# Optimization experiments

Measured on AMD Instinct MI355X. Metric: run time of the kernel, lower is better.

The kernel has to match this reference:

```python
import jax, jax.numpy as jnp
import numpy as np

OUT, IN = 11008, 4096
GROUP = 128
NUM_GROUPS = IN // GROUP  # 32
PACKED = OUT * IN // 2
TOKENS = 4096


def setup_inputs() -> dict:
    key = jax.random.key(0)
    k1, k2, k3, k4 = jax.random.split(key, 4)
    x = jax.random.normal(k1, (TOKENS, IN), dtype=jnp.float32)
    # packed bytes: two int4 values per byte (low nibble = even index)
    w_packed = jax.random.randint(k2, (PACKED,), 0, 256, dtype=jnp.int32)
    # per-(out_channel, group) scale and integer zero-point
    w_scale = jax.random.uniform(k3, (OUT, NUM_GROUPS), dtype=jnp.float32) * 0.02 + 1e-3
    w_zero = jax.random.randint(k4, (OUT, NUM_GROUPS), 0, 16, dtype=jnp.int32)
    return {"x": x, "w_packed": w_packed, "w_scale": w_scale, "w_zero": w_zero}


def _dequant_weight(w_packed, w_scale, w_zero):
    out_features, num_groups = w_scale.shape
    in_features = (w_packed.shape[0] * 2) // out_features
    group = in_features // num_groups
    # unpack nibbles: element 2i -> low nibble, element 2i+1 -> high nibble
    low = w_packed & 15
    high = (w_packed >> 4) & 15
    w4 = jnp.stack([low, high], axis=-1).reshape(out_features, in_features)
    # signed int4: values >= 8 map to value - 16
    w4 = jnp.where(w4 >= 8, w4 - 16, w4).astype(jnp.float32)
    # per-group dequant: (w - zero) * scale
    wg = w4.reshape(out_features, num_groups, group)
    w = (wg - w_zero.astype(jnp.float32)[:, :, None]) * w_scale[:, :, None]
    return w.reshape(out_features, in_features)


def reference(x, w_packed, w_scale, w_zero):
    w = _dequant_weight(w_packed, w_scale, w_zero)  # [OUT, IN]
    return x @ w.T  # [TOKENS, OUT]
```

## Files before the change

kernel.cpp:

```cpp
#include <hip/hip_runtime.h>
#include <hip/hip_bf16.h>
#include <stdint.h>
#include <stddef.h>


#define M_TOK 4096
#define K_IN  4096
#define N_OUT 11008
#define QGROUPS 32

typedef __bf16 bf8 __attribute__((ext_vector_type(8)));
typedef short  s8v __attribute__((ext_vector_type(8)));
typedef float  f4v __attribute__((ext_vector_type(4)));

__device__ __forceinline__ unsigned short f2bf(float f) {
  union { float f; unsigned u; } v; v.f = f;
  unsigned r = v.u + 0x7FFFu + ((v.u >> 16) & 1u);
  return (unsigned short)(r >> 16);
}

__device__ __forceinline__ void gload16(const void* g, void* l) {
  __builtin_amdgcn_global_load_lds(
      (__attribute__((address_space(1))) void*)(g),
      (__attribute__((address_space(3))) void*)(l),
      16, 0, 0);
}

__global__ __launch_bounds__(256) void cvt_x_kernel(const float* __restrict__ x,
                                                    unsigned short* __restrict__ xb) {
  size_t t = (size_t)blockIdx.x * 256 + threadIdx.x;
  const float4* src = (const float4*)x + t * 2;
  float4 a = src[0], b = src[1];
  union { unsigned short u[8]; s8v v; } o;
  o.u[0] = f2bf(a.x); o.u[1] = f2bf(a.y); o.u[2] = f2bf(a.z); o.u[3] = f2bf(a.w);
  o.u[4] = f2bf(b.x); o.u[5] = f2bf(b.y); o.u[6] = f2bf(b.z); o.u[7] = f2bf(b.w);
  ((s8v*)xb)[t] = o.v;
}

__device__ __forceinline__ void deq_pair(int b, float s, float zf, unsigned short* dst) {
  int lo = (b << 28) >> 28;
  int hi = (b << 24) >> 28;
  dst[0] = f2bf(((float)lo - zf) * s);
  dst[1] = f2bf(((float)hi - zf) * s);
}

__global__ __launch_bounds__(256) void deq_w_kernel(const int* __restrict__ wp,
                                                    const float* __restrict__ wsc,
                                                    const int* __restrict__ wz,
                                                    unsigned short* __restrict__ wb) {
  size_t t = (size_t)blockIdx.x * 256 + threadIdx.x;
  size_t e0 = t * 8;
  int o = (int)(e0 >> 12);
  int k = (int)(e0 & 4095);
  int g = k >> 7;
  float s  = wsc[o * QGROUPS + g];
  float zf = (float)wz[o * QGROUPS + g];
  int4 pk = ((const int4*)wp)[t];
  union { unsigned short u[8]; s8v v; } r;
  deq_pair(pk.x, s, zf, &r.u[0]);
  deq_pair(pk.y, s, zf, &r.u[2]);
  deq_pair(pk.z, s, zf, &r.u[4]);
  deq_pair(pk.w, s, zf, &r.u[6]);
  ((s8v*)wb)[t] = r.v;
}

template <bool PRE>
__global__ __launch_bounds__(256, 2) void gemm_kernel(
    const unsigned short* __restrict__ Ab,
    const unsigned short* __restrict__ Bb,
    const float* __restrict__ X,
    const int* __restrict__ WP,
    const float* __restrict__ WS,
    const int* __restrict__ WZ,
    float* __restrict__ C) {
  __shared__ __align__(16) short As[128 * 64];
  __shared__ __align__(16) short Bs[128 * 64];

  const int tid  = threadIdx.x;
  const int lane = tid & 63;
  const int wid  = tid >> 6;
  const int n0 = blockIdx.x * 128;
  const int m0 = blockIdx.y * 128;
  const int wm = (wid >> 1) * 64;
  const int wn = (wid & 1) * 64;
  const int quad = lane >> 4;
  const int lrow = lane & 15;
  const int sw   = lrow & 7;

  f4v acc[4][4];
#pragma unroll
  for (int i = 0; i < 4; ++i)
#pragma unroll
    for (int j = 0; j < 4; ++j) acc[i][j] = (f4v){0.f, 0.f, 0.f, 0.f};

  const int srl = lane >> 3;
  const int skb = (lane & 7) ^ srl;
  const int frow  = tid >> 1;
  const int fhalf = tid & 1;

  for (int kt = 0; kt < K_IN / 64; ++kt) {
    const int k0 = kt * 64;
    __syncthreads();
    if (PRE) {
#pragma unroll
      for (int j = 0; j < 4; ++j) {
        int slab = wid * 4 + j;
        int row  = slab * 8 + srl;
        gload16(Ab + (size_t)(m0 + row) * K_IN + k0 + skb * 8,
                (char*)As + slab * 1024);
        gload16(Bb + (size_t)(n0 + row) * K_IN + k0 + skb * 8,
                (char*)Bs + slab * 1024);
      }
    } else {
      const int g = k0 >> 7;
      float s  = WS[(n0 + frow) * QGROUPS + g];
      float zf = (float)WZ[(n0 + frow) * QGROUPS + g];
#pragma unroll
      for (int j = 0; j < 4; ++j) {
        int kb = fhalf * 4 + j;
        int unit = frow * 8 + (kb ^ (frow & 7));
        const float4* xs = (const float4*)(X + (size_t)(m0 + frow) * K_IN + k0 + kb * 8);
        float4 a = xs[0], b = xs[1];
        union { unsigned short u[8]; s8v v; } oa;
        oa.u[0] = f2bf(a.x); oa.u[1] = f2bf(a.y); oa.u[2] = f2bf(a.z); oa.u[3] = f2bf(a.w);
        oa.u[4] = f2bf(b.x); oa.u[5] = f2bf(b.y); oa.u[6] = f2bf(b.z); oa.u[7] = f2bf(b.w);
        *(s8v*)(As + unit * 8) = oa.v;
        const int4 pk = *(const int4*)(WP + ((size_t)(n0 + frow) * K_IN + k0 + kb * 8) / 2);
        union { unsigned short u[8]; s8v v; } ob;
        deq_pair(pk.x, s, zf, &ob.u[0]);
        deq_pair(pk.y, s, zf, &ob.u[2]);
        deq_pair(pk.z, s, zf, &ob.u[4]);
        deq_pair(pk.w, s, zf, &ob.u[6]);
        *(s8v*)(Bs + unit * 8) = ob.v;
      }
    }
    __syncthreads();

#pragma unroll
    for (int ks = 0; ks < 2; ++ks) {
      bf8 af[4], bfr[4];
#pragma unroll
      for (int mi = 0; mi < 4; ++mi) {
        int row = wm + mi * 16 + lrow;
        int unit = row * 8 + ((ks * 4 + quad) ^ sw);
        af[mi] = *reinterpret_cast<const bf8*>(&As[unit * 8]);
      }
#pragma unroll
      for (int ni = 0; ni < 4; ++ni) {
        int row = wn + ni * 16 + lrow;
        int unit = row * 8 + ((ks * 4 + quad) ^ sw);
        bfr[ni] = *reinterpret_cast<const bf8*>(&Bs[unit * 8]);
      }
#pragma unroll
      for (int mi = 0; mi < 4; ++mi)
#pragma unroll
        for (int ni = 0; ni < 4; ++ni)
          acc[mi][ni] = __builtin_amdgcn_mfma_f32_16x16x32_bf16(
              af[mi], bfr[ni], acc[mi][ni], 0, 0, 0);
    }
  }

#pragma unroll
  for (int mi = 0; mi < 4; ++mi) {
#pragma unroll
    for (int r = 0; r < 4; ++r) {
      int m = m0 + wm + mi * 16 + quad * 4 + r;
      float* crow = C + (size_t)m * N_OUT + n0 + wn + lrow;
#pragma unroll
      for (int ni = 0; ni < 4; ++ni) crow[ni * 16] = acc[mi][ni][r];
    }
  }
}

extern "C" void kernel_launch(void* const* d_in, const int* in_sizes, int n_in,
                              void* d_out, int out_size, void* d_ws, size_t ws_size,
                              hipStream_t stream) {
  const float* x   = (const float*)d_in[0];
  const int*   wp  = (const int*)d_in[1];
  const float* wsc = (const float*)d_in[2];
  const int*   wz  = (const int*)d_in[3];
  float* out = (float*)d_out;

  const size_t needA = (size_t)M_TOK * K_IN * sizeof(unsigned short);
  const size_t needB = (size_t)N_OUT * K_IN * sizeof(unsigned short);
  dim3 grid(N_OUT / 128, M_TOK / 128);

  if (ws_size >= needA + needB) {
    unsigned short* Ab = (unsigned short*)d_ws;
    unsigned short* Bb = (unsigned short*)((char*)d_ws + needA);
    cvt_x_kernel<<<(M_TOK * (size_t)K_IN) / (8 * 256), 256, 0, stream>>>(x, Ab);
    deq_w_kernel<<<((size_t)N_OUT * K_IN) / (8 * 256), 256, 0, stream>>>(wp, wsc, wz, Bb);
    gemm_kernel<true><<<grid, 256, 0, stream>>>(Ab, Bb, nullptr, nullptr, nullptr, nullptr, out);
  } else {
    gemm_kernel<false><<<grid, 256, 0, stream>>>(nullptr, nullptr, x, wp, wsc, wz, out);
  }
}
```

Before: 751.7 us.

## Switch to fp16 MFMA with in-GEMM int4 dequant and grouped tile order

Replaces the bf16 prepass pipeline. Activations are converted to fp16 with a permuted element order, and the weights are repacked into compact 4-bit words instead of a full bf16 dequantized matrix. The GEMM dequantizes the weights in registers using exponent-bias bit tricks (perm plus fma) and software-prefetches the next weight tile. It also remaps block IDs into supertiles for L2 reuse and uses fp16 MFMA. This cuts the large dequantized-weight write and read traffic, at the cost of ALU work inside the GEMM and fp16 range and precision risk.

```diff
diff --git a/kernel.cpp b/kernel.cpp
--- a/kernel.cpp
+++ b/kernel.cpp
@@ -1,5 +1,4 @@
 #include <hip/hip_runtime.h>
-#include <hip/hip_bf16.h>
 #include <stdint.h>
 #include <stddef.h>
 
@@ -8,16 +7,12 @@
 #define K_IN  4096
 #define N_OUT 11008
 #define QGROUPS 32
+#define NBLK (N_OUT / 128)
+#define MBLK (M_TOK / 128)
+#define SUPER (8 * NBLK)
 
-typedef __bf16 bf8 __attribute__((ext_vector_type(8)));
-typedef short  s8v __attribute__((ext_vector_type(8)));
-typedef float  f4v __attribute__((ext_vector_type(4)));
-
-__device__ __forceinline__ unsigned short f2bf(float f) {
-  union { float f; unsigned u; } v; v.f = f;
-  unsigned r = v.u + 0x7FFFu + ((v.u >> 16) & 1u);
-  return (unsigned short)(r >> 16);
-}
+typedef _Float16 h8v __attribute__((ext_vector_type(8)));
+typedef float    f4v __attribute__((ext_vector_type(4)));
 
 __device__ __forceinline__ void gload16(const void* g, void* l) {
   __builtin_amdgcn_global_load_lds(
@@ -27,65 +22,58 @@
 }
 
 __global__ __launch_bounds__(256) void cvt_x_kernel(const float* __restrict__ x,
-                                                    unsigned short* __restrict__ xb) {
+                                                    _Float16* __restrict__ xh) {
   size_t t = (size_t)blockIdx.x * 256 + threadIdx.x;
-  const float4* src = (const float4*)x + t * 2;
-  float4 a = src[0], b = src[1];
-  union { unsigned short u[8]; s8v v; } o;
-  o.u[0] = f2bf(a.x); o.u[1] = f2bf(a.y); o.u[2] = f2bf(a.z); o.u[3] = f2bf(a.w);
-  o.u[4] = f2bf(b.x); o.u[5] = f2bf(b.y); o.u[6] = f2bf(b.z); o.u[7] = f2bf(b.w);
-  ((s8v*)xb)[t] = o.v;
+  const float4* s = (const float4*)x + t * 2;
+  float4 a = s[0], b = s[1];
+  h8v o;
+  o[0] = (_Float16)a.x; o[1] = (_Float16)a.z; o[2] = (_Float16)b.x; o[3] = (_Float16)b.z;
+  o[4] = (_Float16)a.y; o[5] = (_Float16)a.w; o[6] = (_Float16)b.y; o[7] = (_Float16)b.w;
+  ((h8v*)xh)[t] = o;
 }
 
-__device__ __forceinline__ void deq_pair(int b, float s, float zf, unsigned short* dst) {
-  int lo = (b << 28) >> 28;
-  int hi = (b << 24) >> 28;
-  dst[0] = f2bf(((float)lo - zf) * s);
-  dst[1] = f2bf(((float)hi - zf) * s);
+__global__ __launch_bounds__(256) void repack_w_kernel(const int* __restrict__ wp,
+                                                       uint32_t* __restrict__ wq) {
+  size_t t = (size_t)blockIdx.x * 256 + threadIdx.x;
+  const int4* src = (const int4*)wp + t * 4;
+  uint32_t d[4];
+#pragma unroll
+  for (int j = 0; j < 4; ++j) {
+    int4 v = src[j];
+    d[j] = (((uint32_t)v.x & 255u) | (((uint32_t)v.y & 255u) << 8) |
+            (((uint32_t)v.z & 255u) << 16) | (((uint32_t)v.w & 255u) << 24)) ^ 0x88888888u;
+  }
+  uint4 o; o.x = d[0]; o.y = d[1]; o.z = d[2]; o.w = d[3];
+  ((uint4*)wq)[t] = o;
 }
 
-__global__ __launch_bounds__(256) void deq_w_kernel(const int* __restrict__ wp,
-                                                    const float* __restrict__ wsc,
-                                                    const int* __restrict__ wz,
-                                                    unsigned short* __restrict__ wb) {
-  size_t t = (size_t)blockIdx.x * 256 + threadIdx.x;
-  size_t e0 = t * 8;
-  int o = (int)(e0 >> 12);
-  int k = (int)(e0 & 4095);
-  int g = k >> 7;
-  float s  = wsc[o * QGROUPS + g];
-  float zf = (float)wz[o * QGROUPS + g];
-  int4 pk = ((const int4*)wp)[t];
-  union { unsigned short u[8]; s8v v; } r;
-  deq_pair(pk.x, s, zf, &r.u[0]);
-  deq_pair(pk.y, s, zf, &r.u[2]);
-  deq_pair(pk.z, s, zf, &r.u[4]);
-  deq_pair(pk.w, s, zf, &r.u[6]);
-  ((s8v*)wb)[t] = r.v;
-}
-
-template <bool PRE>
 __global__ __launch_bounds__(256, 2) void gemm_kernel(
-    const unsigned short* __restrict__ Ab,
-    const unsigned short* __restrict__ Bb,
-    const float* __restrict__ X,
-    const int* __restrict__ WP,
+    const _Float16* __restrict__ Ah,
+    const uint32_t* __restrict__ Wq,
     const float* __restrict__ WS,
     const int* __restrict__ WZ,
     float* __restrict__ C) {
   __shared__ __align__(16) short As[128 * 64];
   __shared__ __align__(16) short Bs[128 * 64];
 
-  const int tid  = threadIdx.x;
+  const int tid = threadIdx.x;
   const int lane = tid & 63;
-  const int wid  = tid >> 6;
-  const int n0 = blockIdx.x * 128;
-  const int m0 = blockIdx.y * 128;
+  const int wid = tid >> 6;
+  int bid = blockIdx.x;
+  int sup = bid / SUPER;
+  int rem = bid - sup * SUPER;
+  const int m0 = (sup * 8 + (rem & 7)) * 128;
+  const int n0 = (rem >> 3) * 128;
+
   const int wm = (wid >> 1) * 64;
   const int wn = (wid & 1) * 64;
   const int quad = lane >> 4;
   const int lrow = lane & 15;
-  const int sw   = lrow & 7;
+  const int sw = lrow & 7;
+  const int srl = lane >> 3;
+  const int skb = (lane & 7) ^ srl;
+  const int brow = tid >> 1;
+  const int bhalf = tid & 1;
 
   f4v acc[4][4];
 #pragma unroll
@@ -93,70 +81,72 @@
 #pragma unroll
     for (int j = 0; j < 4; ++j) acc[i][j] = (f4v){0.f, 0.f, 0.f, 0.f};
 
-  const int srl = lane >> 3;
-  const int skb = (lane & 7) ^ srl;
-  const int frow  = tid >> 1;
-  const int fhalf = tid & 1;
+  const uint32_t* wrow = Wq + (size_t)(n0 + brow) * (K_IN / 8) + bhalf * 4;
+  const int sbase = (n0 + brow) * QGROUPS;
+
+  uint4 pw = *(const uint4*)wrow;
+  float s = WS[sbase];
+  float zf = (float)WZ[sbase];
 
   for (int kt = 0; kt < K_IN / 64; ++kt) {
     const int k0 = kt * 64;
     __syncthreads();
-    if (PRE) {
+#pragma unroll
+    for (int j = 0; j < 4; ++j) {
+      int slab = wid * 4 + j;
+      int row = slab * 8 + srl;
+      gload16(Ah + (size_t)(m0 + row) * K_IN + k0 + skb * 8,
+              (char*)As + slab * 1024);
+    }
+    {
+      _Float16 sh = (_Float16)s;
+      _Float16 ch = (_Float16)(-s * (136.0f + zf));
+      h8v sv8, cv8;
+#pragma unroll
+      for (int i = 0; i < 8; ++i) { sv8[i] = sh; cv8[i] = ch; }
+      uint32_t wv[4] = {pw.x, pw.y, pw.z, pw.w};
 #pragma unroll
       for (int j = 0; j < 4; ++j) {
-        int slab = wid * 4 + j;
-        int row  = slab * 8 + srl;
-        gload16(Ab + (size_t)(m0 + row) * K_IN + k0 + skb * 8,
-                (char*)As + slab * 1024);
-        gload16(Bb + (size_t)(n0 + row) * K_IN + k0 + skb * 8,
-                (char*)Bs + slab * 1024);
-      }
-    } else {
-      const int g = k0 >> 7;
-      float s  = WS[(n0 + frow) * QGROUPS + g];
-      float zf = (float)WZ[(n0 + frow) * QGROUPS + g];
-#pragma unroll
-      for (int j = 0; j < 4; ++j) {
-        int kb = fhalf * 4 + j;
-        int unit = frow * 8 + (kb ^ (frow & 7));
-        const float4* xs = (const float4*)(X + (size_t)(m0 + frow) * K_IN + k0 + kb * 8);
-        float4 a = xs[0], b = xs[1];
-        union { unsigned short u[8]; s8v v; } oa;
-        oa.u[0] = f2bf(a.x); oa.u[1] = f2bf(a.y); oa.u[2] = f2bf(a.z); oa.u[3] = f2bf(a.w);
-        oa.u[4] = f2bf(b.x); oa.u[5] = f2bf(b.y); oa.u[6] = f2bf(b.z); oa.u[7] = f2bf(b.w);
-        *(s8v*)(As + unit * 8) = oa.v;
-        const int4 pk = *(const int4*)(WP + ((size_t)(n0 + frow) * K_IN + k0 + kb * 8) / 2);
-        union { unsigned short u[8]; s8v v; } ob;
-        deq_pair(pk.x, s, zf, &ob.u[0]);
-        deq_pair(pk.y, s, zf, &ob.u[2]);
-        deq_pair(pk.z, s, zf, &ob.u[4]);
-        deq_pair(pk.w, s, zf, &ob.u[6]);
-        *(s8v*)(Bs + unit * 8) = ob.v;
+        uint32_t w = wv[j];
+        uint32_t ea = (w & 0x0F0F0F0Fu) << 3;
+        uint32_t eb = (w >> 1) & 0x78787878u;
+        union { uint32_t d[4]; h8v v; } u;
+        u.d[0] = __builtin_amdgcn_perm(0x58585858u, ea, 0x04010400u);
+        u.d[1] = __builtin_amdgcn_perm(0x58585858u, ea, 0x04030402u);
+        u.d[2] = __builtin_amdgcn_perm(0x58585858u, eb, 0x04010400u);
+        u.d[3] = __builtin_amdgcn_perm(0x58585858u, eb, 0x04030402u);
+        u.v = __builtin_elementwise_fma(u.v, sv8, cv8);
+        int kb = bhalf * 4 + j;
+        int unit = brow * 8 + (kb ^ (brow & 7));
+        *(h8v*)((char*)Bs + unit * 16) = u.v;
       }
     }
     __syncthreads();
-
+    if (kt < K_IN / 64 - 1) {
+      pw = *(const uint4*)(wrow + (kt + 1) * 8);
+      int g2 = (k0 + 64) >> 7;
+      s = WS[sbase + g2];
+      zf = (float)WZ[sbase + g2];
+    }
 #pragma unroll
     for (int ks = 0; ks < 2; ++ks) {
-      bf8 af[4], bfr[4];
+      h8v af[4], bf[4];
 #pragma unroll
       for (int mi = 0; mi < 4; ++mi) {
-        int row = wm + mi * 16 + lrow;
-        int unit = row * 8 + ((ks * 4 + quad) ^ sw);
-        af[mi] = *reinterpret_cast<const bf8*>(&As[unit * 8]);
+        int unit = (wm + mi * 16 + lrow) * 8 + ((ks * 4 + quad) ^ sw);
+        af[mi] = *(const h8v*)((char*)As + unit * 16);
       }
 #pragma unroll
       for (int ni = 0; ni < 4; ++ni) {
-        int row = wn + ni * 16 + lrow;
-        int unit = row * 8 + ((ks * 4 + quad) ^ sw);
-        bfr[ni] = *reinterpret_cast<const bf8*>(&Bs[unit * 8]);
+        int unit = (wn + ni * 16 + lrow) * 8 + ((ks * 4 + quad) ^ sw);
+        bf[ni] = *(const h8v*)((char*)Bs + unit * 16);
       }
 #pragma unroll
       for (int mi = 0; mi < 4; ++mi)
 #pragma unroll
         for (int ni = 0; ni < 4; ++ni)
-          acc[mi][ni] = __builtin_amdgcn_mfma_f32_16x16x32_bf16(
-              af[mi], bfr[ni], acc[mi][ni], 0, 0, 0);
+          acc[mi][ni] = __builtin_amdgcn_mfma_f32_16x16x32_f16(
+              af[mi], bf[ni], acc[mi][ni], 0, 0, 0);
     }
   }
 
@@ -181,17 +171,10 @@
   const int*   wz  = (const int*)d_in[3];
   float* out = (float*)d_out;
 
-  const size_t needA = (size_t)M_TOK * K_IN * sizeof(unsigned short);
-  const size_t needB = (size_t)N_OUT * K_IN * sizeof(unsigned short);
-  dim3 grid(N_OUT / 128, M_TOK / 128);
+  _Float16* Ah = (_Float16*)d_ws;
+  uint32_t* Wq = (uint32_t*)((char*)d_ws + (size_t)M_TOK * K_IN * 2);
 
-  if (ws_size >= needA + needB) {
-    unsigned short* Ab = (unsigned short*)d_ws;
-    unsigned short* Bb = (unsigned short*)((char*)d_ws + needA);
-    cvt_x_kernel<<<(M_TOK * (size_t)K_IN) / (8 * 256), 256, 0, stream>>>(x, Ab);
-    deq_w_kernel<<<((size_t)N_OUT * K_IN) / (8 * 256), 256, 0, stream>>>(wp, wsc, wz, Bb);
-    gemm_kernel<true><<<grid, 256, 0, stream>>>(Ab, Bb, nullptr, nullptr, nullptr, nullptr, out);
-  } else {
-    gemm_kernel<false><<<grid, 256, 0, stream>>>(nullptr, nullptr, x, wp, wsc, wz, out);
-  }
+  cvt_x_kernel<<<(M_TOK * (size_t)K_IN) / (8 * 256), 256, 0, stream>>>(x, Ah);
+  repack_w_kernel<<<((size_t)N_OUT * K_IN / 2) / (16 * 256), 256, 0, stream>>>(wp, Wq);
+  gemm_kernel<<<MBLK * NBLK, 256, 0, stream>>>(Ah, Wq, wsc, wz, out);
 }
```

Result: slower. 948.9 us (+26.2%).
